# Performance work log

Hardware: AMD Instinct MI355X
Metric: run time of the kernel (lower is better)

The kernel has to match this reference:

```python
import jax, jax.numpy as jnp
from jax import lax
import numpy as np

B, T, D, S, P = 2048, 64, 512, 256, 11
H1 = (D + S) // 2  # position head hidden = (d_model + state_dim)//2 = 384


def setup_inputs() -> dict:
    key = jax.random.key(0)
    ks = jax.random.split(key, 8)
    return {
        "price_features": jax.random.normal(ks[0], (B, T, D), jnp.float32),
        "u": jax.random.uniform(ks[1], (B, T, P), jnp.float32),  # gumbel uniform noise
        "W1": 0.02 * jax.random.normal(ks[2], (H1, D + S), jnp.float32),
        "b1": jnp.zeros((H1,), jnp.float32),
        "W2": 0.02 * jax.random.normal(ks[3], (P, H1), jnp.float32),
        "b2": jnp.zeros((P,), jnp.float32),
        "temperature": jnp.float32(1.0),
        "W_ih": 0.05 * jax.random.normal(ks[4], (3 * S, D + 1), jnp.float32),
        "b_ih": jnp.zeros((3 * S,), jnp.float32),
        "W_hh": 0.05 * jax.random.normal(ks[5], (3 * S, S), jnp.float32),
        "b_hh": jnp.zeros((3 * S,), jnp.float32),
        "h0": jax.random.normal(ks[6], (S,), jnp.float32),  # strategy_state_init
    }


def reference(price_features, u, W1, b1, W2, b2, temperature, W_ih, b_ih, W_hh, b_hh, h0):
    pos_vals = jnp.arange(P, dtype=jnp.float32)
    batch = price_features.shape[0]
    h_init = jnp.broadcast_to(h0, (batch, S))

    def step(h, xs):
        feat, u_t = xs  # feat: [B,D], u_t: [B,P]
        combined = jnp.concatenate([feat, h], axis=-1)          # [B, D+S]
        hidden = jax.nn.relu(combined @ W1.T + b1)              # [B, H1]
        logits = hidden @ W2.T + b2                             # [B, P]
        gumbel = -jnp.log(-jnp.log(u_t + 1e-20) + 1e-20)
        probs = jax.nn.softmax((logits + gumbel) / temperature, axis=-1)
        pos = probs @ pos_vals                                  # [B] expected position
        x = jnp.concatenate([feat, pos[:, None]], axis=-1)      # [B, D+1]
        gi = x @ W_ih.T + b_ih                                  # [B, 3S]
        gh = h @ W_hh.T + b_hh                                  # [B, 3S]
        i_r, i_z, i_n = jnp.split(gi, 3, axis=-1)
        h_r, h_z, h_n = jnp.split(gh, 3, axis=-1)
        r = jax.nn.sigmoid(i_r + h_r)
        z = jax.nn.sigmoid(i_z + h_z)
        n = jnp.tanh(i_n + r * h_n)
        h_new = (1.0 - z) * n + z * h                           # PyTorch GRUCell update
        return h_new, (pos, h_new)

    feats_t = jnp.swapaxes(price_features, 0, 1)  # [T,B,D]
    u_tfirst = jnp.swapaxes(u, 0, 1)              # [T,B,P]
    h_final, (positions, states) = lax.scan(step, h_init, (feats_t, u_tfirst))
    all_expected_positions = jnp.swapaxes(positions, 0, 1)  # [B,T]
    all_strategy_states = jnp.swapaxes(states, 0, 1)        # [B,T,S]
    return all_expected_positions, all_strategy_states, h_final
```

## Files before the change

kernel.cpp:

```cpp
#include <hip/hip_runtime.h>
#include <stdint.h>

#define B_  2048
#define T_  64
#define D_  512
#define S_  256
#define P_  11
#define H1_ 384
#define NG_ 1152
#define KH_ 256

typedef unsigned short ushort_t;
typedef __attribute__((ext_vector_type(4))) float    f32x4;
typedef __attribute__((ext_vector_type(8))) __bf16   bf16x8;
typedef __attribute__((ext_vector_type(8))) unsigned short u16x8;

static __device__ __forceinline__ ushort_t f2bf(float f) {
    uint32_t u = __builtin_bit_cast(uint32_t, f);
    u += 0x7fffu + ((u >> 16) & 1u);
    return (ushort_t)(u >> 16);
}
static __device__ __forceinline__ float bf2f(ushort_t h) {
    uint32_t u = ((uint32_t)h) << 16;
    return __builtin_bit_cast(float, u);
}
static __device__ __forceinline__ u16x8 ntload8(const ushort_t* p) {
    return __builtin_nontemporal_load((const u16x8*)p);
}

__global__ void pack_weights(const float* __restrict__ W1,
                             const float* __restrict__ Wih,
                             const float* __restrict__ Whh,
                             ushort_t* __restrict__ WcatA,
                             ushort_t* __restrict__ WhBp) {
    int idx = blockIdx.x * 256 + threadIdx.x;
    const int tot1 = NG_ * D_;
    if (idx < tot1) {
        int n = idx >> 9;
        int k = idx & 511;
        float v = (n < H1_) ? W1[n * 768 + k] : Wih[(n - H1_) * 513 + k];
        WcatA[idx] = f2bf(v);
    } else {
        int i = idx - tot1;
        int j  = i & 7;
        int l  = (i >> 3) & 63;
        int kc = (i >> 9) & 7;
        int nt = i >> 12;
        int row = nt * 16 + (l & 15);
        int col = kc * 32 + (l >> 4) * 8 + j;
        float v = (row < H1_) ? W1[row * 768 + 512 + col] : Whh[(row - H1_) * 256 + col];
        WhBp[i] = f2bf(v);
    }
}

__global__ __launch_bounds__(256) void gemm_pre(
        const float* __restrict__ feat,
        const ushort_t* __restrict__ WcatA,
        ushort_t* __restrict__ pre) {
    __shared__ __attribute__((aligned(16))) ushort_t Asub[128][72];
    __shared__ __attribute__((aligned(16))) ushort_t Bsub[128][72];

    int bx = blockIdx.x;
    int xcd = bx & 7, slot = bx >> 3;
    int mt = (slot / 9) * 8 + xcd;
    int ntb = slot % 9;
    int m0 = mt * 128, n0 = ntb * 128;

    int tid = threadIdx.x;
    int lane = tid & 63, wave = tid >> 6;
    int wr = wave >> 1, wc = wave & 1;
    int l15 = lane & 15, q = lane >> 4;

    f32x4 acc[4][4];
    #pragma unroll
    for (int i = 0; i < 4; ++i)
        #pragma unroll
        for (int j = 0; j < 4; ++j)
            acc[i][j] = (f32x4){0.f, 0.f, 0.f, 0.f};

    for (int kt = 0; kt < 8; ++kt) {
        int kbase = kt * 64;
        #pragma unroll
        for (int r = 0; r < 4; ++r) {
            int c = tid + 256 * r;
            int row = c >> 3, sub = c & 7;
            const float* gp = feat + (size_t)(m0 + row) * 512 + kbase + sub * 8;
            f32x4 f0 = *(const f32x4*)gp;
            f32x4 f1 = *(const f32x4*)(gp + 4);
            u16x8 o;
            #pragma unroll
            for (int j = 0; j < 4; ++j) { o[j] = f2bf(f0[j]); o[4 + j] = f2bf(f1[j]); }
            *(u16x8*)&Asub[row][sub * 8] = o;
        }
        #pragma unroll
        for (int r = 0; r < 4; ++r) {
            int c = tid + 256 * r;
            int row = c >> 3, sub = c & 7;
            u16x8 w = *(const u16x8*)(WcatA + (size_t)(n0 + row) * 512 + kbase + sub * 8);
            *(u16x8*)&Bsub[row][sub * 8] = w;
        }
        __syncthreads();
        #pragma unroll
        for (int kc = 0; kc < 2; ++kc) {
            bf16x8 af[4], bfr[4];
            #pragma unroll
            for (int i = 0; i < 4; ++i)
                af[i] = __builtin_bit_cast(bf16x8,
                    *(const u16x8*)&Asub[wr * 64 + i * 16 + l15][kc * 32 + q * 8]);
            #pragma unroll
            for (int j = 0; j < 4; ++j)
                bfr[j] = __builtin_bit_cast(bf16x8,
                    *(const u16x8*)&Bsub[wc * 64 + j * 16 + l15][kc * 32 + q * 8]);
            #pragma unroll
            for (int i = 0; i < 4; ++i)
                #pragma unroll
                for (int j = 0; j < 4; ++j)
                    acc[i][j] = __builtin_amdgcn_mfma_f32_16x16x32_bf16(
                        af[i], bfr[j], acc[i][j], 0, 0, 0);
        }
        __syncthreads();
    }
    #pragma unroll
    for (int i = 0; i < 4; ++i) {
        #pragma unroll
        for (int r = 0; r < 4; ++r) {
            int m = m0 + wr * 64 + i * 16 + q * 4 + r;
            int orow = (m & 63) * 2048 + (m >> 6);
            ushort_t* op = pre + (size_t)orow * NG_ + n0 + wc * 64 + l15;
            #pragma unroll
            for (int j = 0; j < 4; ++j)
                __builtin_nontemporal_store(f2bf(acc[i][j][r]), &op[j * 16]);
        }
    }
}

__global__ __launch_bounds__(1024, 4) void recurrent(
        const float* __restrict__ u,
        const float* __restrict__ b1,
        const float* __restrict__ W2,
        const float* __restrict__ b2,
        const float* __restrict__ temp_p,
        const float* __restrict__ Wih,
        const float* __restrict__ bih,
        const float* __restrict__ bhh,
        const float* __restrict__ h0,
        const ushort_t* __restrict__ WhBp,
        const ushort_t* __restrict__ pre,
        float* __restrict__ out_pos,
        float* __restrict__ out_states,
        float* __restrict__ out_hfin) {
    __shared__ __attribute__((aligned(16))) ushort_t gates[8][1160];
    __shared__ __attribute__((aligned(16))) ushort_t preg[8][1160];
    __shared__ __attribute__((aligned(16))) float    hf[8][256];
    __shared__ __attribute__((aligned(16))) ushort_t hb[16][264];
    __shared__ __attribute__((aligned(16))) ushort_t hidb[16][392];
    __shared__ __attribute__((aligned(16))) ushort_t w2s[16][392];
    __shared__ __attribute__((aligned(16))) float    b1s[384];
    __shared__ __attribute__((aligned(16))) float    wps[768];
    __shared__ __attribute__((aligned(16))) float    bihs[768];
    __shared__ __attribute__((aligned(16))) float    bhhs[768];
    __shared__ float    b2s[16];
    __shared__ float    logit_s[8][17];
    __shared__ float    pos_s[8];
    __shared__ float    u_s[8][12];

    const int tid  = threadIdx.x;
    const int lane = tid & 63, wave = tid >> 6;
    const int l15  = lane & 15, q = lane >> 4;
    const int row8 = tid >> 7;
    const int ln128 = tid & 127;
    const int b0 = blockIdx.x * 8;

    for (int i = tid; i < 384; i += 1024) b1s[i] = b1[i];
    for (int i = tid; i < 768; i += 1024) {
        wps[i]  = Wih[i * 513 + 512];
        bihs[i] = bih[i];
        bhhs[i] = bhh[i];
    }
    if (tid < 11) b2s[tid] = b2[tid];
    for (int i = tid; i < 16 * 392; i += 1024) {
        int r = i / 392, c = i - r * 392;
        float v = (r < 11 && c < 384) ? W2[r * 384 + c] : 0.f;
        w2s[r][c] = f2bf(v);
    }
    for (int i = tid; i < 8 * 256; i += 1024) {
        int m = i >> 8, s = i & 255;
        float v = h0[s];
        hf[m][s] = v;
        hb[m][s] = f2bf(v);
    }
    for (int i = tid; i < 8 * 264; i += 1024) {
        int m = 8 + i / 264;
        hb[m][i % 264] = 0;
    }
    for (int i = tid; i < 8 * 392; i += 1024) {
        int m = 8 + i / 392;
        hidb[m][i % 392] = 0;
    }
    float tinv = 1.0f / temp_p[0];

    u16x8 pr[2];
    {
        const size_t prow = (size_t)b0;
        #pragma unroll
        for (int r = 0; r < 2; ++r) {
            int c = tid + (r << 10);
            if (c < 1152) {
                int row = c / 144, off = c - row * 144;
                pr[r] = ntload8(pre + (prow + row) * NG_ + (size_t)off * 8);
            }
        }
    }
    float uval = 0.f;
    const int um = tid / 11, up = tid - um * 11;
    if (tid < 88) uval = u[((size_t)(b0 + um) * 64 + 0) * 11 + up];
    __syncthreads();

    for (int t = 0; t < 64; ++t) {
        #pragma unroll
        for (int r = 0; r < 2; ++r) {
            int c = tid + (r << 10);
            if (c < 1152) {
                int row = c / 144, off = c - row * 144;
                *(u16x8*)&preg[row][off * 8] = pr[r];
            }
        }
        if (tid < 88) u_s[um][up] = uval;

        bf16x8 af[8];
        #pragma unroll
        for (int kc = 0; kc < 8; ++kc)
            af[kc] = __builtin_bit_cast(bf16x8, *(const u16x8*)&hb[l15][kc * 32 + q * 8]);

        for (int nt = wave; nt < 24; nt += 16) {
            f32x4 acc = (f32x4){0.f, 0.f, 0.f, 0.f};
            const ushort_t* wp = WhBp + (((size_t)nt * 8) << 9) + (lane << 3);
            #pragma unroll
            for (int kc = 0; kc < 8; ++kc) {
                bf16x8 bfr = __builtin_bit_cast(bf16x8, *(const u16x8*)(wp + ((size_t)kc << 9)));
                acc = __builtin_amdgcn_mfma_f32_16x16x32_bf16(af[kc], bfr, acc, 0, 0, 0);
            }
            if (q < 2) {
                int n = nt * 16 + l15;
                #pragma unroll
                for (int r = 0; r < 4; ++r)
                    gates[q * 4 + r][n] = f2bf(acc[r]);
            }
        }
        __syncthreads();

        if (ln128 < 48) {
            int c = ln128 << 3;
            u16x8 g8 = *(const u16x8*)&gates[row8][c];
            u16x8 p8 = *(const u16x8*)&preg[row8][c];
            f32x4 ba = *(const f32x4*)&b1s[c];
            f32x4 bb = *(const f32x4*)&b1s[c + 4];
            u16x8 o;
            #pragma unroll
            for (int jj = 0; jj < 8; ++jj) {
                float bv = (jj < 4) ? ba[jj] : bb[jj - 4];
                float v = bf2f(g8[jj]) + bf2f(p8[jj]) + bv;
                o[jj] = f2bf(fmaxf(v, 0.f));
            }
            *(u16x8*)&hidb[row8][c] = o;
        }
        __syncthreads();

        if (wave == 0) {
            f32x4 lacc = (f32x4){0.f, 0.f, 0.f, 0.f};
            #pragma unroll
            for (int kc = 0; kc < 12; ++kc) {
                bf16x8 ha = __builtin_bit_cast(bf16x8,
                    *(const u16x8*)&hidb[l15][kc * 32 + q * 8]);
                bf16x8 wb = __builtin_bit_cast(bf16x8,
                    *(const u16x8*)&w2s[l15][kc * 32 + q * 8]);
                lacc = __builtin_amdgcn_mfma_f32_16x16x32_bf16(ha, wb, lacc, 0, 0, 0);
            }
            if (q < 2) {
                #pragma unroll
                for (int r = 0; r < 4; ++r)
                    logit_s[q * 4 + r][l15] = lacc[r];
            }
            __builtin_amdgcn_s_waitcnt(0);
            if (lane < 8) {
                int m = lane;
                float lg[11];
                float mx = -1e30f;
                #pragma unroll
                for (int p = 0; p < 11; ++p) {
                    float uu = u_s[m][p];
                    float g = -__logf(-__logf(uu + 1e-20f) + 1e-20f);
                    float a = (logit_s[m][p] + b2s[p] + g) * tinv;
                    lg[p] = a;
                    mx = fmaxf(mx, a);
                }
                float se = 0.f, sp = 0.f;
                #pragma unroll
                for (int p = 0; p < 11; ++p) {
                    float e = __expf(lg[p] - mx);
                    se += e;
                    sp += e * (float)p;
                }
                float pos = sp / se;
                pos_s[m] = pos;
                __builtin_nontemporal_store(pos, &out_pos[(size_t)(b0 + m) * 64 + t]);
            }
        } else {
            for (int nt = 23 + wave; nt < 72; nt += 15) {
                f32x4 acc = (f32x4){0.f, 0.f, 0.f, 0.f};
                const ushort_t* wp = WhBp + (((size_t)nt * 8) << 9) + (lane << 3);
                #pragma unroll
                for (int kc = 0; kc < 8; ++kc) {
                    bf16x8 bfr = __builtin_bit_cast(bf16x8, *(const u16x8*)(wp + ((size_t)kc << 9)));
                    acc = __builtin_amdgcn_mfma_f32_16x16x32_bf16(af[kc], bfr, acc, 0, 0, 0);
                }
                if (q < 2) {
                    int n = nt * 16 + l15;
                    #pragma unroll
                    for (int r = 0; r < 4; ++r)
                        gates[q * 4 + r][n] = f2bf(acc[r]);
                }
            }
        }

        if (t < 63) {
            const size_t prow = (size_t)(t + 1) * 2048 + b0;
            #pragma unroll
            for (int r = 0; r < 2; ++r) {
                int c = tid + (r << 10);
                if (c < 1152) {
                    int row = c / 144, off = c - row * 144;
                    pr[r] = ntload8(pre + (prow + row) * NG_ + (size_t)off * 8);
                }
            }
            if (tid < 88) uval = u[((size_t)(b0 + um) * 64 + (t + 1)) * 11 + up];
        }
        __syncthreads();

        {
            float pos = pos_s[row8];
            float* st = out_states + ((size_t)(b0 + row8) * 64 + t) * 256;
            #pragma unroll
            for (int j = 0; j < 2; ++j) {
                int s = ln128 + (j << 7);
                float ar  = bf2f(preg[row8][384 + s]) + bihs[s]
                          + bf2f(gates[row8][384 + s]) + bhhs[s];
                float az  = bf2f(preg[row8][640 + s]) + bihs[256 + s]
                          + bf2f(gates[row8][640 + s]) + bhhs[256 + s];
                float in0 = bf2f(preg[row8][896 + s]) + bihs[512 + s];
                float gn  = bf2f(gates[row8][896 + s]) + bhhs[512 + s];
                float hp  = hf[row8][s];
                float rr = __builtin_amdgcn_rcpf(1.f + __expf(-(ar + pos * wps[s])));
                float zz = __builtin_amdgcn_rcpf(1.f + __expf(-(az + pos * wps[256 + s])));
                float xn = in0 + pos * wps[512 + s] + rr * gn;
                float e2 = __expf(2.f * xn);
                float nn = 1.f - 2.f * __builtin_amdgcn_rcpf(e2 + 1.f);
                float hnew = (1.f - zz) * nn + zz * hp;
                hf[row8][s] = hnew;
                hb[row8][s] = f2bf(hnew);
                __builtin_nontemporal_store(hnew, st + s);
            }
        }
        __syncthreads();
    }

    for (int i = tid; i < 8 * 256; i += 1024) {
        int m = i >> 8, s = i & 255;
        __builtin_nontemporal_store(hf[m][s], &out_hfin[(size_t)(b0 + m) * 256 + s]);
    }
}

extern "C" void kernel_launch(void* const* d_in, const int* in_sizes, int n_in,
                              void* d_out, int out_size, void* d_ws, size_t ws_size,
                              hipStream_t stream) {
    const float* feat = (const float*)d_in[0];
    const float* u    = (const float*)d_in[1];
    const float* W1   = (const float*)d_in[2];
    const float* b1   = (const float*)d_in[3];
    const float* W2   = (const float*)d_in[4];
    const float* b2   = (const float*)d_in[5];
    const float* temp = (const float*)d_in[6];
    const float* Wih  = (const float*)d_in[7];
    const float* bih  = (const float*)d_in[8];
    const float* Whh  = (const float*)d_in[9];
    const float* bhh  = (const float*)d_in[10];
    const float* h0   = (const float*)d_in[11];

    ushort_t* WcatA = (ushort_t*)d_ws;
    ushort_t* WhBp  = WcatA + NG_ * D_;
    ushort_t* pre   = WhBp + NG_ * KH_;

    float* out_pos    = (float*)d_out;
    float* out_states = out_pos + (size_t)B_ * T_;
    float* out_hfin   = out_states + (size_t)B_ * T_ * S_;

    pack_weights<<<3456, 256, 0, stream>>>(W1, Wih, Whh, WcatA, WhBp);
    gemm_pre<<<9216, 256, 0, stream>>>(feat, WcatA, pre);
    recurrent<<<256, 1024, 0, stream>>>(u, b1, W2, b2, temp, Wih, bih, bhh, h0,
                                        WhBp, pre, out_pos, out_states, out_hfin);
}
```

Before: 1.098 ms.

## Pre-convert features to swizzled bf16 tiles and load GEMM operands via global_load_lds

After: 1.107 ms. Within noise of the previous version (+0.8%).

```diff
diff --git a/kernel.cpp b/kernel.cpp
--- a/kernel.cpp
+++ b/kernel.cpp
@@ -27,19 +27,52 @@
 static __device__ __forceinline__ u16x8 ntload8(const ushort_t* p) {
     return __builtin_nontemporal_load((const u16x8*)p);
 }
+static __device__ __forceinline__ void gload16(const ushort_t* g, ushort_t* l) {
+    __builtin_amdgcn_global_load_lds(
+        (const __attribute__((address_space(1))) uint32_t*)(const void*)g,
+        (__attribute__((address_space(3))) uint32_t*)(void*)l,
+        16, 0, 0);
+}
+
+
+__global__ __launch_bounds__(256) void convert_feat(
+        const float* __restrict__ feat,
+        ushort_t* __restrict__ featS) {
+    int base = blockIdx.x * 1024 + threadIdx.x;
+    #pragma unroll
+    for (int k = 0; k < 4; ++k) {
+        int o = base + k * 256;
+        int tile = o >> 10;
+        int s = o & 1023;
+        int row = s >> 3, slot = s & 7;
+        int mtile = tile >> 3, kt = tile & 7;
+        int col = kt * 64 + (((slot ^ (row & 7))) << 3);
+        const float* gp = feat + (size_t)(mtile * 128 + row) * 512 + col;
+        f32x4 f0 = *(const f32x4*)gp;
+        f32x4 f1 = *(const f32x4*)(gp + 4);
+        u16x8 ov;
+        #pragma unroll
+        for (int j = 0; j < 4; ++j) { ov[j] = f2bf(f0[j]); ov[4 + j] = f2bf(f1[j]); }
+        __builtin_nontemporal_store(ov, (u16x8*)(featS + (size_t)o * 8));
+    }
+}
 
 __global__ void pack_weights(const float* __restrict__ W1,
                              const float* __restrict__ Wih,
                              const float* __restrict__ Whh,
-                             ushort_t* __restrict__ WcatA,
+                             ushort_t* __restrict__ WcatS,
                              ushort_t* __restrict__ WhBp) {
     int idx = blockIdx.x * 256 + threadIdx.x;
     const int tot1 = NG_ * D_;
     if (idx < tot1) {
-        int n = idx >> 9;
-        int k = idx & 511;
-        float v = (n < H1_) ? W1[n * 768 + k] : Wih[(n - H1_) * 513 + k];
-        WcatA[idx] = f2bf(v);
+        int tile = idx >> 13;
+        int e = idx & 8191;
+        int row = e >> 6, slot = (e >> 3) & 7, j = e & 7;
+        int ntile = tile >> 3, kt = tile & 7;
+        int col = kt * 64 + ((slot ^ (row & 7)) << 3) + j;
+        int n = ntile * 128 + row;
+        float v = (n < H1_) ? W1[n * 768 + col] : Wih[(n - H1_) * 513 + col];
+        WcatS[idx] = f2bf(v);
     } else {
         int i = idx - tot1;
         int j  = i & 7;
@@ -54,16 +87,16 @@
 }
 
 __global__ __launch_bounds__(256) void gemm_pre(
-        const float* __restrict__ feat,
-        const ushort_t* __restrict__ WcatA,
+        const ushort_t* __restrict__ featS,
+        const ushort_t* __restrict__ WcatS,
         ushort_t* __restrict__ pre) {
-    __shared__ __attribute__((aligned(16))) ushort_t Asub[128][72];
-    __shared__ __attribute__((aligned(16))) ushort_t Bsub[128][72];
+    __shared__ __attribute__((aligned(16))) ushort_t As[8192];
+    __shared__ __attribute__((aligned(16))) ushort_t Bs[8192];
 
     int bx = blockIdx.x;
-    int xcd = bx & 7, slot = bx >> 3;
-    int mt = (slot / 9) * 8 + xcd;
-    int ntb = slot % 9;
+    int xcd = bx & 7, slt = bx >> 3;
+    int mt = (slt / 9) * 8 + xcd;
+    int ntb = slt % 9;
     int m0 = mt * 128, n0 = ntb * 128;
 
     int tid = threadIdx.x;
@@ -71,6 +104,9 @@
     int wr = wave >> 1, wc = wave & 1;
     int l15 = lane & 15, q = lane >> 4;
 
+    const ushort_t* Abase = featS + (size_t)mt * 8 * 8192 + (size_t)(lane << 3);
+    const ushort_t* Bbase = WcatS + (size_t)ntb * 8 * 8192 + (size_t)(lane << 3);
+
     f32x4 acc[4][4];
     #pragma unroll
     for (int i = 0; i < 4; ++i)
@@ -78,39 +114,28 @@
         for (int j = 0; j < 4; ++j)
             acc[i][j] = (f32x4){0.f, 0.f, 0.f, 0.f};
 
+    const int swz = (l15 & 7) << 4;
+
     for (int kt = 0; kt < 8; ++kt) {
-        int kbase = kt * 64;
-        #pragma unroll
-        for (int r = 0; r < 4; ++r) {
-            int c = tid + 256 * r;
-            int row = c >> 3, sub = c & 7;
-            const float* gp = feat + (size_t)(m0 + row) * 512 + kbase + sub * 8;
-            f32x4 f0 = *(const f32x4*)gp;
-            f32x4 f1 = *(const f32x4*)(gp + 4);
-            u16x8 o;
-            #pragma unroll
-            for (int j = 0; j < 4; ++j) { o[j] = f2bf(f0[j]); o[4 + j] = f2bf(f1[j]); }
-            *(u16x8*)&Asub[row][sub * 8] = o;
-        }
-        #pragma unroll
-        for (int r = 0; r < 4; ++r) {
-            int c = tid + 256 * r;
-            int row = c >> 3, sub = c & 7;
-            u16x8 w = *(const u16x8*)(WcatA + (size_t)(n0 + row) * 512 + kbase + sub * 8);
-            *(u16x8*)&Bsub[row][sub * 8] = w;
+        #pragma unroll
+        for (int i = 0; i < 4; ++i) {
+            int c = wave * 4 + i;
+            gload16(Abase + (size_t)kt * 8192 + (c << 9), &As[c << 9]);
+            gload16(Bbase + (size_t)kt * 8192 + (c << 9), &Bs[c << 9]);
         }
         __syncthreads();
         #pragma unroll
         for (int kc = 0; kc < 2; ++kc) {
+            const int coff = (kc * 64 + q * 16) ^ swz;
             bf16x8 af[4], bfr[4];
             #pragma unroll
             for (int i = 0; i < 4; ++i)
-                af[i] = __builtin_bit_cast(bf16x8,
-                    *(const u16x8*)&Asub[wr * 64 + i * 16 + l15][kc * 32 + q * 8]);
+                af[i] = __builtin_bit_cast(bf16x8, *(const u16x8*)(
+                    (const char*)As + (wr * 64 + i * 16 + l15) * 128 + coff));
             #pragma unroll
             for (int j = 0; j < 4; ++j)
-                bfr[j] = __builtin_bit_cast(bf16x8,
-                    *(const u16x8*)&Bsub[wc * 64 + j * 16 + l15][kc * 32 + q * 8]);
+                bfr[j] = __builtin_bit_cast(bf16x8, *(const u16x8*)(
+                    (const char*)Bs + (wc * 64 + j * 16 + l15) * 128 + coff));
             #pragma unroll
             for (int i = 0; i < 4; ++i)
                 #pragma unroll
@@ -386,16 +411,18 @@
     const float* bhh  = (const float*)d_in[10];
     const float* h0   = (const float*)d_in[11];
 
-    ushort_t* WcatA = (ushort_t*)d_ws;
-    ushort_t* WhBp  = WcatA + NG_ * D_;
+    ushort_t* WcatS = (ushort_t*)d_ws;
+    ushort_t* WhBp  = WcatS + NG_ * D_;
     ushort_t* pre   = WhBp + NG_ * KH_;
+    ushort_t* featS = pre + (size_t)T_ * B_ * NG_;
 
     float* out_pos    = (float*)d_out;
     float* out_states = out_pos + (size_t)B_ * T_;
     float* out_hfin   = out_states + (size_t)B_ * T_ * S_;
 
-    pack_weights<<<3456, 256, 0, stream>>>(W1, Wih, Whh, WcatA, WhBp);
-    gemm_pre<<<9216, 256, 0, stream>>>(feat, WcatA, pre);
+    pack_weights<<<3456, 256, 0, stream>>>(W1, Wih, Whh, WcatS, WhBp);
+    convert_feat<<<8192, 256, 0, stream>>>(feat, featS);
+    gemm_pre<<<9216, 256, 0, stream>>>(featS, WcatS, pre);
     recurrent<<<256, 1024, 0, stream>>>(u, b1, W2, b2, temp, Wih, bih, bhh, h0,
                                         WhBp, pre, out_pos, out_states, out_hfin);
 }
```
